# Kernel optimization log

Hardware: AMD Instinct MI355X
Metric: run time of the kernel (lower is better)

Reference implementation:

```python
import jax, jax.numpy as jnp
import numpy as np

DIM = 512
NUM_HEADS = 8
HEAD_DIM = DIM // NUM_HEADS
SCALE = HEAD_DIM ** -0.5
B, N, K_HOPS = 16, 1024, 5


def setup_inputs() -> dict:
    key = jax.random.key(0)
    ks = jax.random.split(key, 7)
    x = jax.random.normal(ks[0], (B, N, DIM), jnp.float32)
    Hstack = jax.random.uniform(ks[1], (K_HOPS, N, N), jnp.float32)
    hop_logits_attn = jax.random.normal(ks[2], (NUM_HEADS, K_HOPS), jnp.float32)
    rel_alpha = jax.random.normal(ks[3], (NUM_HEADS,), jnp.float32)
    Wqkv = jax.random.normal(ks[4], (3 * DIM, DIM), jnp.float32) * 0.02
    Wproj = jax.random.normal(ks[5], (DIM, DIM), jnp.float32) * 0.02
    bproj = jax.random.normal(ks[6], (DIM,), jnp.float32) * 0.02
    return {"x": x, "Hstack": Hstack, "hop_logits_attn": hop_logits_attn,
            "rel_alpha": rel_alpha, "Wqkv": Wqkv, "Wproj": Wproj, "bproj": bproj}


def reference(x, Hstack, hop_logits_attn, rel_alpha, Wqkv, Wproj, bproj):
    bs, n_tok, c_dim = x.shape
    # qkv projection: [B,N,3C] -> [3,B,H,N,hd]
    qkv = (x @ Wqkv.T).reshape(bs, n_tok, 3, NUM_HEADS, c_dim // NUM_HEADS)
    qkv = qkv.transpose(2, 0, 3, 1, 4)
    q, k, v = qkv[0], qkv[1], qkv[2]
    logits = jnp.einsum('bhnd,bhmd->bhnm', q, k) * SCALE  # [B,H,N,N]
    # hop-distance bias: per-head softmax mixture over K hop matrices
    w = jax.nn.softmax(hop_logits_attn, axis=-1)          # [H,K]
    B_head = jnp.einsum('hk,kij->hij', w, Hstack)          # [H,N,N]
    attn_bias = rel_alpha[:, None, None] * B_head          # [H,N,N]
    attn = jax.nn.softmax(logits + attn_bias[None], axis=-1)
    out = jnp.einsum('bhnm,bhmd->bhnd', attn, v)           # [B,H,N,hd]
    out = out.transpose(0, 2, 1, 3).reshape(bs, n_tok, c_dim)
    return out @ Wproj.T + bproj
```

## Files before the change

kernel.cpp:

```cpp
#include <hip/hip_runtime.h>
#include <hip/hip_bf16.h>
#include <hip/hip_fp16.h>
#include <stdint.h>

#define DIM   512
#define NH    8
#define HD    64
#define NB    16
#define NTOK  1024
#define KHOPS 5

typedef __attribute__((ext_vector_type(8))) short bf16x8;
typedef __attribute__((ext_vector_type(4))) float f32x4;

#define LOG2E 1.4426950408889634f

__device__ __forceinline__ unsigned short f32_to_bf16(float f) {
    unsigned int u = __builtin_bit_cast(unsigned int, f);
    unsigned int r = (u + 0x7FFFu + ((u >> 16) & 1u)) >> 16;
    return (unsigned short)r;
}

__device__ __forceinline__ float fast_exp2(float x) {
    return __builtin_amdgcn_exp2f(x);
}

#define AS1C(p) ((const __attribute__((address_space(1))) void*)(p))
#define AS3(p)  ((__attribute__((address_space(3))) void*)(p))

__global__ __launch_bounds__(256) void cvt_all(const float* __restrict__ x,
                                               const float* __restrict__ wq,
                                               const float* __restrict__ wp,
                                               unsigned short* __restrict__ xb,
                                               unsigned short* __restrict__ wqb,
                                               unsigned short* __restrict__ wpb) {
    int bid = blockIdx.x;
    const float* in; unsigned short* out; int i;
    if (bid < 8192)      { in = x;  out = xb;  i = bid * 256 + threadIdx.x; }
    else if (bid < 8960) { in = wq; out = wqb; i = (bid - 8192) * 256 + threadIdx.x; }
    else                 { in = wp; out = wpb; i = (bid - 8960) * 256 + threadIdx.x; }
    float4 v = reinterpret_cast<const float4*>(in)[i];
    ushort4 o;
    o.x = f32_to_bf16(v.x); o.y = f32_to_bf16(v.y);
    o.z = f32_to_bf16(v.z); o.w = f32_to_bf16(v.w);
    reinterpret_cast<ushort4*>(out)[i] = o;
}

__global__ __launch_bounds__(256) void bias_fused(const float* __restrict__ H,
                                                  const float* __restrict__ hop_logits,
                                                  const float* __restrict__ rel_alpha,
                                                  uint32_t* __restrict__ biast) {
    __shared__ unsigned short Ls[64 * 76];
    const int tid = threadIdx.x;
    const int jt = blockIdx.x, it = blockIdx.y, h = blockIdx.z;
    const int j0 = jt * 64, i0 = it * 64;
    float cf[KHOPS];
    {
        float m = -1e30f;
#pragma unroll
        for (int k = 0; k < KHOPS; ++k) m = fmaxf(m, hop_logits[h * KHOPS + k]);
        float s = 0.f;
#pragma unroll
        for (int k = 0; k < KHOPS; ++k) { cf[k] = fast_exp2((hop_logits[h * KHOPS + k] - m) * LOG2E); s += cf[k]; }
        float ra = rel_alpha[h] * LOG2E / s;
#pragma unroll
        for (int k = 0; k < KHOPS; ++k) cf[k] *= ra;
    }
    const int r = tid >> 2, c0 = (tid & 3) * 16;
    float acc[16];
#pragma unroll
    for (int e = 0; e < 16; ++e) acc[e] = 0.f;
    for (int k = 0; k < KHOPS; ++k) {
        const float4* src = reinterpret_cast<const float4*>(
            H + (size_t)k * 1048576 + (size_t)(i0 + r) * 1024 + j0 + c0);
#pragma unroll
        for (int q = 0; q < 4; ++q) {
            float4 v = src[q];
            acc[q * 4 + 0] += cf[k] * v.x; acc[q * 4 + 1] += cf[k] * v.y;
            acc[q * 4 + 2] += cf[k] * v.z; acc[q * 4 + 3] += cf[k] * v.w;
        }
    }
#pragma unroll
    for (int q = 0; q < 4; ++q) {
        __half2 p0 = __floats2half2_rn(acc[q * 4 + 0], acc[q * 4 + 1]);
        __half2 p1 = __floats2half2_rn(acc[q * 4 + 2], acc[q * 4 + 3]);
        uint32_t* d = reinterpret_cast<uint32_t*>(&Ls[r * 76 + c0 + q * 4]);
        d[0] = __builtin_bit_cast(uint32_t, p0);
        d[1] = __builtin_bit_cast(uint32_t, p1);
    }
    __syncthreads();
    const int iw2 = tid & 15, jl = tid >> 4;
#pragma unroll
    for (int g = 0; g < 2; ++g)
#pragma unroll
        for (int t = 0; t < 4; ++t) {
            int j = t * 16 + jl;
            int i = g * 32 + iw2 * 2;
            uint32_t lo = (uint32_t)Ls[i * 76 + j] | ((uint32_t)Ls[(i + 1) * 76 + j] << 16);
            biast[(size_t)((h * 32 + (i0 >> 5) + g) * 1024 + (j0 + j)) * 16 + iw2] = lo;
        }
}

__global__ __launch_bounds__(256) void gemm_qkv(const unsigned short* __restrict__ A,
                                                const unsigned short* __restrict__ Bw,
                                                unsigned short* __restrict__ qkv,
                                                unsigned short* __restrict__ vt) {
    __shared__ unsigned short As[128 * 32];
    __shared__ unsigned short Bs[128 * 32];
    const int tid  = threadIdx.x;
    const int lane = tid & 63;
    const int w    = tid >> 6;
    const int wr   = (w >> 1) * 64, wc = (w & 1) * 64;
    const int l15  = lane & 15, quad = lane >> 4;
    const int m0   = blockIdx.x * 128, n0 = blockIdx.y * 128;
    const int K = 512, Nn = 1536;

    f32x4 acc[4][4];
#pragma unroll
    for (int i = 0; i < 4; ++i)
#pragma unroll
        for (int j = 0; j < 4; ++j) { acc[i][j][0] = 0.f; acc[i][j][1] = 0.f; acc[i][j][2] = 0.f; acc[i][j][3] = 0.f; }

    for (int k0 = 0; k0 < K; k0 += 32) {
        __syncthreads();
#pragma unroll
        for (int t = 0; t < 2; ++t) {
            int c = t * 256 + w * 64 + lane;
            int r = c >> 2, kh = c & 3;
            const unsigned short* ga = A  + (size_t)(m0 + r) * K + k0 + kh * 8;
            const unsigned short* gb = Bw + (size_t)(n0 + r) * K + k0 + kh * 8;
            __builtin_amdgcn_global_load_lds(AS1C(ga), AS3(&As[(t * 256 + w * 64) * 8]), 16, 0, 0);
            __builtin_amdgcn_global_load_lds(AS1C(gb), AS3(&Bs[(t * 256 + w * 64) * 8]), 16, 0, 0);
        }
        __syncthreads();
        bf16x8 af[4], bfr[4];
#pragma unroll
        for (int rt = 0; rt < 4; ++rt)
            af[rt] = *reinterpret_cast<const bf16x8*>(&As[(wr + rt * 16 + l15) * 32 + quad * 8]);
#pragma unroll
        for (int ct = 0; ct < 4; ++ct)
            bfr[ct] = *reinterpret_cast<const bf16x8*>(&Bs[(wc + ct * 16 + l15) * 32 + quad * 8]);
#pragma unroll
        for (int rt = 0; rt < 4; ++rt)
#pragma unroll
            for (int ct = 0; ct < 4; ++ct)
                acc[rt][ct] = __builtin_amdgcn_mfma_f32_16x16x32_bf16(af[rt], bfr[ct], acc[rt][ct], 0, 0, 0);
    }

    if (n0 < 1024) {
#pragma unroll
        for (int rt = 0; rt < 4; ++rt)
#pragma unroll
            for (int ct = 0; ct < 4; ++ct)
#pragma unroll
                for (int reg = 0; reg < 4; ++reg) {
                    int row = m0 + wr + rt * 16 + quad * 4 + reg;
                    int col = n0 + wc + ct * 16 + l15;
                    qkv[(size_t)row * Nn + col] = f32_to_bf16(acc[rt][ct][reg]);
                }
    } else {
        const int b = m0 >> 10;
#pragma unroll
        for (int ct = 0; ct < 4; ++ct) {
            int c = n0 - 1024 + wc + ct * 16 + l15;
            unsigned short* vrow = vt + ((size_t)(b * 8) * 64 + c) * 1024;
#pragma unroll
            for (int rt = 0; rt < 4; ++rt) {
                int trow = (m0 & 1023) + wr + rt * 16 + quad * 4;
                ushort4 pk;
                pk.x = f32_to_bf16(acc[rt][ct][0]);
                pk.y = f32_to_bf16(acc[rt][ct][1]);
                pk.z = f32_to_bf16(acc[rt][ct][2]);
                pk.w = f32_to_bf16(acc[rt][ct][3]);
                *reinterpret_cast<ushort4*>(vrow + trow) = pk;
            }
        }
    }
}

__global__ __launch_bounds__(256) void gemm_proj(const unsigned short* __restrict__ A,
                                                 const unsigned short* __restrict__ Bw,
                                                 float* __restrict__ C,
                                                 const float* __restrict__ cbias,
                                                 int M, int Nn, int K) {
    __shared__ unsigned short As[128 * 32];
    __shared__ unsigned short Bs[128 * 32];
    const int tid  = threadIdx.x;
    const int lane = tid & 63;
    const int w    = tid >> 6;
    const int wr   = (w >> 1) * 64, wc = (w & 1) * 64;
    const int l15  = lane & 15, quad = lane >> 4;
    const int m0   = blockIdx.x * 128, n0 = blockIdx.y * 128;

    f32x4 acc[4][4];
#pragma unroll
    for (int i = 0; i < 4; ++i)
#pragma unroll
        for (int j = 0; j < 4; ++j) { acc[i][j][0] = 0.f; acc[i][j][1] = 0.f; acc[i][j][2] = 0.f; acc[i][j][3] = 0.f; }

    for (int k0 = 0; k0 < K; k0 += 32) {
        __syncthreads();
#pragma unroll
        for (int t = 0; t < 2; ++t) {
            int c = t * 256 + w * 64 + lane;
            int r = c >> 2, kh = c & 3;
            const unsigned short* ga = A  + (size_t)(m0 + r) * K + k0 + kh * 8;
            const unsigned short* gb = Bw + (size_t)(n0 + r) * K + k0 + kh * 8;
            __builtin_amdgcn_global_load_lds(AS1C(ga), AS3(&As[(t * 256 + w * 64) * 8]), 16, 0, 0);
            __builtin_amdgcn_global_load_lds(AS1C(gb), AS3(&Bs[(t * 256 + w * 64) * 8]), 16, 0, 0);
        }
        __syncthreads();
        bf16x8 af[4], bfr[4];
#pragma unroll
        for (int rt = 0; rt < 4; ++rt)
            af[rt] = *reinterpret_cast<const bf16x8*>(&As[(wr + rt * 16 + l15) * 32 + quad * 8]);
#pragma unroll
        for (int ct = 0; ct < 4; ++ct)
            bfr[ct] = *reinterpret_cast<const bf16x8*>(&Bs[(wc + ct * 16 + l15) * 32 + quad * 8]);
#pragma unroll
        for (int rt = 0; rt < 4; ++rt)
#pragma unroll
            for (int ct = 0; ct < 4; ++ct)
                acc[rt][ct] = __builtin_amdgcn_mfma_f32_16x16x32_bf16(af[rt], bfr[ct], acc[rt][ct], 0, 0, 0);
    }

#pragma unroll
    for (int ct = 0; ct < 4; ++ct) {
        int col = n0 + wc + ct * 16 + l15;
        float bv = cbias[col];
#pragma unroll
        for (int rt = 0; rt < 4; ++rt)
#pragma unroll
            for (int reg = 0; reg < 4; ++reg) {
                int row = m0 + wr + rt * 16 + quad * 4 + reg;
                C[(size_t)row * Nn + col] = acc[rt][ct][reg] + bv;
            }
    }
}

__global__ __launch_bounds__(256, 3) void flash_attn(const unsigned short* __restrict__ qkv,
                                                     const unsigned short* __restrict__ vt,
                                                     const unsigned short* __restrict__ biast,
                                                     unsigned short* __restrict__ aout) {
    __shared__ unsigned short Kb[64 * 64];
    __shared__ unsigned short Vb[64 * 64];
    __shared__ unsigned short Ps[4 * 32 * 72];
    const int tid  = threadIdx.x;
    const int lane = tid & 63, w = tid >> 6;
    const int l15  = lane & 15, quad = lane >> 4;
    const int h = blockIdx.x, qt = blockIdx.y, b = blockIdx.z;
    const int i0 = qt * 128 + w * 32;
    const float kscale = 0.125f * LOG2E;
    const int l7 = l15 & 7;

    bf16x8 qf[2][2];
#pragma unroll
    for (int rt = 0; rt < 2; ++rt)
#pragma unroll
        for (int ks = 0; ks < 2; ++ks)
            qf[rt][ks] = *reinterpret_cast<const bf16x8*>(
                qkv + (size_t)(b * 1024 + i0 + rt * 16 + l15) * 1536 + h * 64 + ks * 32 + quad * 8);

    f32x4 o[2][4];
    f32x4 lacc[2];
#pragma unroll
    for (int rt = 0; rt < 2; ++rt) {
#pragma unroll
        for (int nt = 0; nt < 4; ++nt) { o[rt][nt][0] = 0.f; o[rt][nt][1] = 0.f; o[rt][nt][2] = 0.f; o[rt][nt][3] = 0.f; }
        lacc[rt][0] = 0.f; lacc[rt][1] = 0.f; lacc[rt][2] = 0.f; lacc[rt][3] = 0.f;
    }

    bf16x8 ones;
#pragma unroll
    for (int e = 0; e < 8; ++e) ones[e] = (short)0x3F80;

    const int srow = lane >> 3;
    const int gch  = (lane & 7) ^ (srow & 7);
    const unsigned short* kgbase = qkv + (size_t)b * 1024 * 1536 + 512 + h * 64 + gch * 8;
    const unsigned short* vgbase = vt + (size_t)((b * 8 + h) * 64) * 1024 + gch * 8;
    const unsigned short* bb = biast + ((size_t)(h * 32 + qt * 4 + w) * 1024) * 32 + quad * 4;
    unsigned short* ps = &Ps[w * 32 * 72];

    for (int j0 = 0; j0 < 1024; j0 += 64) {
        __syncthreads();
#pragma unroll
        for (int t = 0; t < 2; ++t) {
            int rl = w * 16 + t * 8 + srow;
            __builtin_amdgcn_global_load_lds(AS1C(kgbase + (size_t)(j0 + rl) * 1536),
                                             AS3(&Kb[(w * 16 + t * 8) * 64]), 16, 0, 0);
            __builtin_amdgcn_global_load_lds(AS1C(vgbase + (size_t)rl * 1024 + j0),
                                             AS3(&Vb[(w * 16 + t * 8) * 64]), 16, 0, 0);
        }
        uint2 bl[2][4];
#pragma unroll
        for (int rt = 0; rt < 2; ++rt)
#pragma unroll
            for (int jt = 0; jt < 4; ++jt)
                bl[rt][jt] = *reinterpret_cast<const uint2*>(
                    bb + (size_t)(j0 + jt * 16 + l15) * 32 + rt * 16);
        __syncthreads();

        f32x4 s[2][4];
#pragma unroll
        for (int rt = 0; rt < 2; ++rt)
#pragma unroll
            for (int jt = 0; jt < 4; ++jt) { s[rt][jt][0] = 0.f; s[rt][jt][1] = 0.f; s[rt][jt][2] = 0.f; s[rt][jt][3] = 0.f; }
#pragma unroll
        for (int ks = 0; ks < 2; ++ks) {
            bf16x8 kf[4];
#pragma unroll
            for (int jt = 0; jt < 4; ++jt)
                kf[jt] = *reinterpret_cast<const bf16x8*>(
                    &Kb[(jt * 16 + l15) * 64 + (((ks * 4 + quad) ^ l7) * 8)]);
#pragma unroll
            for (int rt = 0; rt < 2; ++rt)
#pragma unroll
                for (int jt = 0; jt < 4; ++jt)
                    s[rt][jt] = __builtin_amdgcn_mfma_f32_16x16x32_bf16(qf[rt][ks], kf[jt], s[rt][jt], 0, 0, 0);
        }

#pragma unroll
        for (int rt = 0; rt < 2; ++rt)
#pragma unroll
            for (int jt = 0; jt < 4; ++jt) {
                float2 f0 = __half22float2(__builtin_bit_cast(__half2, bl[rt][jt].x));
                float2 f1 = __half22float2(__builtin_bit_cast(__half2, bl[rt][jt].y));
                float bvr[4] = {f0.x, f0.y, f1.x, f1.y};
#pragma unroll
                for (int reg = 0; reg < 4; ++reg) {
                    float p = fast_exp2(__builtin_fmaf(s[rt][jt][reg], kscale, bvr[reg]));
                    ps[(rt * 16 + quad * 4 + reg) * 72 + jt * 16 + l15] = f32_to_bf16(p);
                }
            }

#pragma unroll
        for (int ks = 0; ks < 2; ++ks) {
            bf16x8 pf[2], vf[4];
#pragma unroll
            for (int rt = 0; rt < 2; ++rt)
                pf[rt] = *reinterpret_cast<const bf16x8*>(ps + (rt * 16 + l15) * 72 + ks * 32 + quad * 8);
#pragma unroll
            for (int nt = 0; nt < 4; ++nt)
                vf[nt] = *reinterpret_cast<const bf16x8*>(
                    &Vb[(nt * 16 + l15) * 64 + (((ks * 4 + quad) ^ l7) * 8)]);
#pragma unroll
            for (int rt = 0; rt < 2; ++rt) {
#pragma unroll
                for (int nt = 0; nt < 4; ++nt)
                    o[rt][nt] = __builtin_amdgcn_mfma_f32_16x16x32_bf16(pf[rt], vf[nt], o[rt][nt], 0, 0, 0);
                lacc[rt] = __builtin_amdgcn_mfma_f32_16x16x32_bf16(pf[rt], ones, lacc[rt], 0, 0, 0);
            }
        }
    }

#pragma unroll
    for (int rt = 0; rt < 2; ++rt) {
        float inv[4];
#pragma unroll
        for (int reg = 0; reg < 4; ++reg) inv[reg] = 1.f / lacc[rt][reg];
#pragma unroll
        for (int nt = 0; nt < 4; ++nt)
#pragma unroll
            for (int reg = 0; reg < 4; ++reg) {
                int row = b * 1024 + i0 + rt * 16 + quad * 4 + reg;
                int col = h * 64 + nt * 16 + l15;
                aout[(size_t)row * 512 + col] = f32_to_bf16(o[rt][nt][reg] * inv[reg]);
            }
    }
}

extern "C" void kernel_launch(void* const* d_in, const int* in_sizes, int n_in,
                              void* d_out, int out_size, void* d_ws, size_t ws_size,
                              hipStream_t stream) {
    const float* x          = (const float*)d_in[0];
    const float* Hstack     = (const float*)d_in[1];
    const float* hop_logits = (const float*)d_in[2];
    const float* rel_alpha  = (const float*)d_in[3];
    const float* Wqkv       = (const float*)d_in[4];
    const float* Wproj      = (const float*)d_in[5];
    const float* bproj      = (const float*)d_in[6];
    float* out = (float*)d_out;

    char* ws = (char*)d_ws;
    unsigned short* xb    = (unsigned short*)(ws);
    unsigned short* wqb   = (unsigned short*)(ws + 16777216);
    unsigned short* wpb   = (unsigned short*)(ws + 18350080);
    unsigned short* qkvb  = (unsigned short*)(ws + 18874368);
    unsigned short* vtb   = (unsigned short*)(ws + 69206016);
    unsigned short* biast = (unsigned short*)(ws + 85983232);
    unsigned short* aoutb = (unsigned short*)(ws + 102760448);

    cvt_all<<<9216, 256, 0, stream>>>(x, Wqkv, Wproj, xb, wqb, wpb);

    bias_fused<<<dim3(16, 16, 8), 256, 0, stream>>>(Hstack, hop_logits, rel_alpha, (uint32_t*)biast);

    gemm_qkv<<<dim3(128, 12), 256, 0, stream>>>(xb, wqb, qkvb, vtb);

    flash_attn<<<dim3(8, 8, 16), 256, 0, stream>>>(qkvb, vtb, biast, aoutb);

    gemm_proj<<<dim3(128, 4), 256, 0, stream>>>(aoutb, wpb, out, bproj, 16384, 512, 512);
}
```

Before: 255.2 us.

## Double-buffer attention K/V tiles, share Hstack reads across heads, remap GEMM blocks per XCD

The flash attention kernel now double-buffers its K and V shared-memory tiles, prefetching the next tile while computing the current one, and drops one barrier per iteration. The bias kernel reads each Hstack tile once and produces all eight heads from it, cutting Hstack global traffic eightfold at the cost of more registers and a serial loop over heads. Both GEMMs use a 1D grid that maps consecutive M tiles to the same XCD for better L2 reuse. The K/V swizzle expression was also simplified, which is equivalent since srow is already below 8.

```diff
diff --git a/kernel.cpp b/kernel.cpp
--- a/kernel.cpp
+++ b/kernel.cpp
@@ -52,53 +52,64 @@
                                                   uint32_t* __restrict__ biast) {
     __shared__ unsigned short Ls[64 * 76];
     const int tid = threadIdx.x;
-    const int jt = blockIdx.x, it = blockIdx.y, h = blockIdx.z;
+    const int jt = blockIdx.x, it = blockIdx.y;
     const int j0 = jt * 64, i0 = it * 64;
-    float cf[KHOPS];
-    {
+    float cf[NH][KHOPS];
+#pragma unroll
+    for (int h = 0; h < NH; ++h) {
         float m = -1e30f;
 #pragma unroll
         for (int k = 0; k < KHOPS; ++k) m = fmaxf(m, hop_logits[h * KHOPS + k]);
         float s = 0.f;
 #pragma unroll
-        for (int k = 0; k < KHOPS; ++k) { cf[k] = fast_exp2((hop_logits[h * KHOPS + k] - m) * LOG2E); s += cf[k]; }
+        for (int k = 0; k < KHOPS; ++k) { cf[h][k] = fast_exp2((hop_logits[h * KHOPS + k] - m) * LOG2E); s += cf[h][k]; }
         float ra = rel_alpha[h] * LOG2E / s;
 #pragma unroll
-        for (int k = 0; k < KHOPS; ++k) cf[k] *= ra;
+        for (int k = 0; k < KHOPS; ++k) cf[h][k] *= ra;
     }
     const int r = tid >> 2, c0 = (tid & 3) * 16;
-    float acc[16];
-#pragma unroll
-    for (int e = 0; e < 16; ++e) acc[e] = 0.f;
+    float hv[KHOPS][16];
+#pragma unroll
     for (int k = 0; k < KHOPS; ++k) {
         const float4* src = reinterpret_cast<const float4*>(
             H + (size_t)k * 1048576 + (size_t)(i0 + r) * 1024 + j0 + c0);
 #pragma unroll
         for (int q = 0; q < 4; ++q) {
             float4 v = src[q];
-            acc[q * 4 + 0] += cf[k] * v.x; acc[q * 4 + 1] += cf[k] * v.y;
-            acc[q * 4 + 2] += cf[k] * v.z; acc[q * 4 + 3] += cf[k] * v.w;
-        }
-    }
-#pragma unroll
-    for (int q = 0; q < 4; ++q) {
-        __half2 p0 = __floats2half2_rn(acc[q * 4 + 0], acc[q * 4 + 1]);
-        __half2 p1 = __floats2half2_rn(acc[q * 4 + 2], acc[q * 4 + 3]);
-        uint32_t* d = reinterpret_cast<uint32_t*>(&Ls[r * 76 + c0 + q * 4]);
-        d[0] = __builtin_bit_cast(uint32_t, p0);
-        d[1] = __builtin_bit_cast(uint32_t, p1);
-    }
-    __syncthreads();
+            hv[k][q * 4 + 0] = v.x; hv[k][q * 4 + 1] = v.y;
+            hv[k][q * 4 + 2] = v.z; hv[k][q * 4 + 3] = v.w;
+        }
+    }
     const int iw2 = tid & 15, jl = tid >> 4;
-#pragma unroll
-    for (int g = 0; g < 2; ++g)
-#pragma unroll
-        for (int t = 0; t < 4; ++t) {
-            int j = t * 16 + jl;
-            int i = g * 32 + iw2 * 2;
-            uint32_t lo = (uint32_t)Ls[i * 76 + j] | ((uint32_t)Ls[(i + 1) * 76 + j] << 16);
-            biast[(size_t)((h * 32 + (i0 >> 5) + g) * 1024 + (j0 + j)) * 16 + iw2] = lo;
-        }
+    for (int h = 0; h < NH; ++h) {
+#pragma unroll
+        for (int q = 0; q < 4; ++q) {
+            float a0 = 0.f, a1 = 0.f, a2 = 0.f, a3 = 0.f;
+#pragma unroll
+            for (int k = 0; k < KHOPS; ++k) {
+                a0 += cf[h][k] * hv[k][q * 4 + 0];
+                a1 += cf[h][k] * hv[k][q * 4 + 1];
+                a2 += cf[h][k] * hv[k][q * 4 + 2];
+                a3 += cf[h][k] * hv[k][q * 4 + 3];
+            }
+            __half2 p0 = __floats2half2_rn(a0, a1);
+            __half2 p1 = __floats2half2_rn(a2, a3);
+            uint32_t* d = reinterpret_cast<uint32_t*>(&Ls[r * 76 + c0 + q * 4]);
+            d[0] = __builtin_bit_cast(uint32_t, p0);
+            d[1] = __builtin_bit_cast(uint32_t, p1);
+        }
+        __syncthreads();
+#pragma unroll
+        for (int g = 0; g < 2; ++g)
+#pragma unroll
+            for (int t = 0; t < 4; ++t) {
+                int j = t * 16 + jl;
+                int i = g * 32 + iw2 * 2;
+                uint32_t lo = (uint32_t)Ls[i * 76 + j] | ((uint32_t)Ls[(i + 1) * 76 + j] << 16);
+                biast[(size_t)((h * 32 + (i0 >> 5) + g) * 1024 + (j0 + j)) * 16 + iw2] = lo;
+            }
+        __syncthreads();
+    }
 }
 
 __global__ __launch_bounds__(256) void gemm_qkv(const unsigned short* __restrict__ A,
@@ -112,7 +123,10 @@
     const int w    = tid >> 6;
     const int wr   = (w >> 1) * 64, wc = (w & 1) * 64;
     const int l15  = lane & 15, quad = lane >> 4;
-    const int m0   = blockIdx.x * 128, n0 = blockIdx.y * 128;
+    const int bid  = blockIdx.x;
+    const int xcd  = bid & 7, slot = bid >> 3;
+    const int m0   = (xcd * 16 + (slot & 15)) * 128;
+    const int n0   = (slot >> 4) * 128;
     const int K = 512, Nn = 1536;
 
     f32x4 acc[4][4];
@@ -181,8 +195,7 @@
 __global__ __launch_bounds__(256) void gemm_proj(const unsigned short* __restrict__ A,
                                                  const unsigned short* __restrict__ Bw,
                                                  float* __restrict__ C,
-                                                 const float* __restrict__ cbias,
-                                                 int M, int Nn, int K) {
+                                                 const float* __restrict__ cbias) {
     __shared__ unsigned short As[128 * 32];
     __shared__ unsigned short Bs[128 * 32];
     const int tid  = threadIdx.x;
@@ -190,7 +203,11 @@
     const int w    = tid >> 6;
     const int wr   = (w >> 1) * 64, wc = (w & 1) * 64;
     const int l15  = lane & 15, quad = lane >> 4;
-    const int m0   = blockIdx.x * 128, n0 = blockIdx.y * 128;
+    const int bid  = blockIdx.x;
+    const int xcd  = bid & 7, slot = bid >> 3;
+    const int m0   = (xcd * 16 + (slot & 15)) * 128;
+    const int n0   = (slot >> 4) * 128;
+    const int K = 512, Nn = 512;
 
     f32x4 acc[4][4];
 #pragma unroll
@@ -242,8 +259,8 @@
                                                      const unsigned short* __restrict__ vt,
                                                      const unsigned short* __restrict__ biast,
                                                      unsigned short* __restrict__ aout) {
-    __shared__ unsigned short Kb[64 * 64];
-    __shared__ unsigned short Vb[64 * 64];
+    __shared__ unsigned short Kb[2][64 * 64];
+    __shared__ unsigned short Vb[2][64 * 64];
     __shared__ unsigned short Ps[4 * 32 * 72];
     const int tid  = threadIdx.x;
     const int lane = tid & 63, w = tid >> 6;
@@ -275,22 +292,39 @@
     for (int e = 0; e < 8; ++e) ones[e] = (short)0x3F80;
 
     const int srow = lane >> 3;
-    const int gch  = (lane & 7) ^ (srow & 7);
+    const int gch  = (lane & 7) ^ srow;
     const unsigned short* kgbase = qkv + (size_t)b * 1024 * 1536 + 512 + h * 64 + gch * 8;
     const unsigned short* vgbase = vt + (size_t)((b * 8 + h) * 64) * 1024 + gch * 8;
     const unsigned short* bb = biast + ((size_t)(h * 32 + qt * 4 + w) * 1024) * 32 + quad * 4;
     unsigned short* ps = &Ps[w * 32 * 72];
 
-    for (int j0 = 0; j0 < 1024; j0 += 64) {
-        __syncthreads();
-#pragma unroll
-        for (int t = 0; t < 2; ++t) {
-            int rl = w * 16 + t * 8 + srow;
-            __builtin_amdgcn_global_load_lds(AS1C(kgbase + (size_t)(j0 + rl) * 1536),
-                                             AS3(&Kb[(w * 16 + t * 8) * 64]), 16, 0, 0);
-            __builtin_amdgcn_global_load_lds(AS1C(vgbase + (size_t)rl * 1024 + j0),
-                                             AS3(&Vb[(w * 16 + t * 8) * 64]), 16, 0, 0);
-        }
+#pragma unroll
+    for (int t = 0; t < 2; ++t) {
+        int rl = w * 16 + t * 8 + srow;
+        __builtin_amdgcn_global_load_lds(AS1C(kgbase + (size_t)rl * 1536),
+                                         AS3(&Kb[0][(w * 16 + t * 8) * 64]), 16, 0, 0);
+        __builtin_amdgcn_global_load_lds(AS1C(vgbase + (size_t)rl * 1024),
+                                         AS3(&Vb[0][(w * 16 + t * 8) * 64]), 16, 0, 0);
+    }
+
+#pragma unroll 2
+    for (int it = 0; it < 16; ++it) {
+        const int cur = it & 1, nxt = cur ^ 1;
+        const int j0 = it * 64;
+        __syncthreads();
+
+        if (it < 15) {
+            const int j0n = j0 + 64;
+#pragma unroll
+            for (int t = 0; t < 2; ++t) {
+                int rl = w * 16 + t * 8 + srow;
+                __builtin_amdgcn_global_load_lds(AS1C(kgbase + (size_t)(j0n + rl) * 1536),
+                                                 AS3(&Kb[nxt][(w * 16 + t * 8) * 64]), 16, 0, 0);
+                __builtin_amdgcn_global_load_lds(AS1C(vgbase + (size_t)rl * 1024 + j0n),
+                                                 AS3(&Vb[nxt][(w * 16 + t * 8) * 64]), 16, 0, 0);
+            }
+        }
+
         uint2 bl[2][4];
 #pragma unroll
         for (int rt = 0; rt < 2; ++rt)
@@ -298,7 +332,6 @@
             for (int jt = 0; jt < 4; ++jt)
                 bl[rt][jt] = *reinterpret_cast<const uint2*>(
                     bb + (size_t)(j0 + jt * 16 + l15) * 32 + rt * 16);
-        __syncthreads();
 
         f32x4 s[2][4];
 #pragma unroll
@@ -311,7 +344,7 @@
 #pragma unroll
             for (int jt = 0; jt < 4; ++jt)
                 kf[jt] = *reinterpret_cast<const bf16x8*>(
-                    &Kb[(jt * 16 + l15) * 64 + (((ks * 4 + quad) ^ l7) * 8)]);
+                    &Kb[cur][(jt * 16 + l15) * 64 + (((ks * 4 + quad) ^ l7) * 8)]);
 #pragma unroll
             for (int rt = 0; rt < 2; ++rt)
 #pragma unroll
@@ -342,7 +375,7 @@
 #pragma unroll
             for (int nt = 0; nt < 4; ++nt)
                 vf[nt] = *reinterpret_cast<const bf16x8*>(
-                    &Vb[(nt * 16 + l15) * 64 + (((ks * 4 + quad) ^ l7) * 8)]);
+                    &Vb[cur][(nt * 16 + l15) * 64 + (((ks * 4 + quad) ^ l7) * 8)]);
 #pragma unroll
             for (int rt = 0; rt < 2; ++rt) {
 #pragma unroll
@@ -392,11 +425,11 @@
 
     cvt_all<<<9216, 256, 0, stream>>>(x, Wqkv, Wproj, xb, wqb, wpb);
 
-    bias_fused<<<dim3(16, 16, 8), 256, 0, stream>>>(Hstack, hop_logits, rel_alpha, (uint32_t*)biast);
-
-    gemm_qkv<<<dim3(128, 12), 256, 0, stream>>>(xb, wqb, qkvb, vtb);
+    bias_fused<<<dim3(16, 16), 256, 0, stream>>>(Hstack, hop_logits, rel_alpha, (uint32_t*)biast);
+
+    gemm_qkv<<<1536, 256, 0, stream>>>(xb, wqb, qkvb, vtb);
 
     flash_attn<<<dim3(8, 8, 16), 256, 0, stream>>>(qkvb, vtb, biast, aoutb);
 
-    gemm_proj<<<dim3(128, 4), 256, 0, stream>>>(aoutb, wpb, out, bproj, 16384, 512, 512);
-}
+    gemm_proj<<<512, 256, 0, stream>>>(aoutb, wpb, out, bproj);
+}
```

After: 241.1 us. 5.5% less time.
